# Kernel optimization log

Measured on AMD Instinct MI355X. Metric: run time of the kernel, lower is better.

The kernel has to match this reference:

```python
import jax, jax.numpy as jnp
import numpy as np

B, A, E, H = 512, 4, 10, 256
OBS, PHY, G, MV = 2, 3, 3, 2
T = 10
STEP = 0.05


def setup_inputs() -> dict:
    key = jax.random.key(0)
    ks = jax.random.split(key, 16)
    rn = lambda k, s, sc=1.0: jax.random.normal(k, s, jnp.float32) * sc
    W = 0.1  # weight scale so tanh/sigmoid stay in sane range
    return {
        'observations': rn(ks[0], (B, A, E, OBS)),
        'physical': rn(ks[1], (B, E, PHY)),
        'observed_goals': rn(ks[2], (B, A, G)),
        'mem_physical': jnp.zeros((B, A, E, H), jnp.float32),
        'mem_action': jnp.zeros((B, A, H), jnp.float32),
        'W_ih_p': rn(ks[3], (3 * H, OBS + PHY), W),
        'W_hh_p': rn(ks[4], (3 * H, H), W),
        'b_ih_p': jnp.zeros((3 * H,), jnp.float32),
        'b_hh_p': jnp.zeros((3 * H,), jnp.float32),
        'W_fc_p': rn(ks[5], (H, H), W),
        'b_fc_p': jnp.zeros((H,), jnp.float32),
        'W_ih_a': rn(ks[6], (3 * H, H + G), W),
        'W_hh_a': rn(ks[7], (3 * H, H), W),
        'b_ih_a': jnp.zeros((3 * H,), jnp.float32),
        'b_hh_a': jnp.zeros((3 * H,), jnp.float32),
        'W_fc_a': rn(ks[8], (H, H), W),
        'b_fc_a': jnp.zeros((H,), jnp.float32),
        'W_m1': rn(ks[9], (H, H), W),
        'b_m1': jnp.zeros((H,), jnp.float32),
        'W_m2': rn(ks[10], (MV, H), W),
        'b_m2': jnp.zeros((MV,), jnp.float32),
    }


def _gru(x, h, Wih, Whh, bih, bhh):
    # torch.nn.GRUCell math, vectorized over leading dims
    gi = x @ Wih.T + bih
    gh = h @ Whh.T + bhh
    ir, iz, inn = jnp.split(gi, 3, axis=-1)
    hr, hz, hn = jnp.split(gh, 3, axis=-1)
    r = jax.nn.sigmoid(ir + hr)
    z = jax.nn.sigmoid(iz + hz)
    n = jnp.tanh(inn + r * hn)
    return (1.0 - z) * n + z * h


def reference(observations, physical, observed_goals, mem_physical, mem_action,
              W_ih_p, W_hh_p, b_ih_p, b_hh_p, W_fc_p, b_fc_p,
              W_ih_a, W_hh_a, b_ih_a, b_hh_a, W_fc_a, b_fc_a,
              W_m1, b_m1, W_m2, b_m2):
    b, a, e, _ = observations.shape
    # per-(agent, entity) input: cat(observation, entity physical features)
    phys_b = jnp.broadcast_to(physical[:, None], (b, a, e, physical.shape[-1]))
    x_p = jnp.concatenate([observations, phys_b], axis=-1)  # [B,A,E,5]

    def step(carry, _):
        mp, ma = carry  # [B,A,E,H], [B,A,H]
        # physical ProcessingModule over all (agent, entity) pairs at once
        h_p = _gru(x_p, mp, W_ih_p, W_hh_p, b_ih_p, b_hh_p)          # new 'physical' memory
        proc = jax.nn.elu(h_p @ W_fc_p.T + b_fc_p)                    # [B,A,E,H]
        feat = jnp.max(proc, axis=2)                                  # AdaptiveMaxPool2d((1,H)) over entities
        # ActionModule: GRU over cat(pooled physical feat, observed goal)
        x_a = jnp.concatenate([feat, observed_goals], axis=-1)       # [B,A,H+G]
        h_a = _gru(x_a, ma, W_ih_a, W_hh_a, b_ih_a, b_hh_a)          # new 'action' memory
        proc_a = jax.nn.elu(h_a @ W_fc_a.T + b_fc_a)
        mv = jnp.tanh(jax.nn.elu(proc_a @ W_m1.T + b_m1) @ W_m2.T + b_m2) * STEP  # [B,A,MV]
        return (h_p, h_a), mv

    _, movements = jax.lax.scan(step, (mem_physical, mem_action), None, length=T)
    return movements  # [T,B,A,MV]
```

## Files before the change

kernel.cpp:

```cpp
#include <hip/hip_runtime.h>
#include <math.h>

#define H 256
#define G3 768
#define BB 512
#define AA 4
#define EE 10
#define RP (BB*AA*EE)
#define RA (BB*AA)
#define TT 10
#define NMV 2
#define STEPSC 0.05f
#define DST 260
#define A1B 128
#define A2B 256
#define A3B 128
#define COMB 1280

typedef __attribute__((ext_vector_type(8))) short short8;
typedef __attribute__((ext_vector_type(8))) _Float16 half8;
typedef __attribute__((ext_vector_type(4))) float f32x4;

#if defined(__has_builtin)
#  if __has_builtin(__builtin_amdgcn_global_load_lds)
#    define HAS_GLL 1
#  endif
#endif

__device__ __forceinline__ float sigmoid_(float x){ return 1.f/(1.f + __expf(-x)); }
__device__ __forceinline__ float tanh_(float x){
    float ax = fabsf(x);
    float e  = __expf(-2.f*ax);
    float t  = (1.f - e)/(1.f + e);
    return copysignf(t, x);
}
__device__ __forceinline__ float elu_(float x){ return x > 0.f ? x : (__expf(x) - 1.f); }

#define MFMA16(A,B,C) __builtin_amdgcn_mfma_f32_16x16x32_f16(A,B,C,0,0,0)

__device__ __forceinline__ void cp16(const void* g, void* l) {
#ifdef HAS_GLL
    __builtin_amdgcn_global_load_lds(
        (const __attribute__((address_space(1))) unsigned int*)g,
        (__attribute__((address_space(3))) unsigned int*)l, 16, 0, 0);
#else
    *(short8*)l = *(const short8*)g;
#endif
}

__global__ void k_splitw(const float* __restrict__ src, _Float16* __restrict__ dst,
                         int n, int ldsrc)
{
    int i = blockIdx.x*256 + threadIdx.x;
    if (i < n) {
        int j  = i & 7;
        int l  = (i >> 3) & 63;
        int kc = (i >> 9) & 7;
        int c  = i >> 12;
        int row = c*16 + (l & 15);
        int k   = kc*32 + (l >> 4)*8 + j;
        dst[i] = (_Float16)src[(size_t)row*ldsrc + k];
    }
}

__global__ void k_gia_goal(const float* __restrict__ goals,
                           const float* __restrict__ Wiha,
                           const float* __restrict__ biha,
                           _Float16* __restrict__ out)
{
    int idx = blockIdx.x*256 + threadIdx.x;
    int ra = idx / G3, k = idx % G3;
    float g0 = goals[ra*3+0], g1 = goals[ra*3+1], g2 = goals[ra*3+2];
    const float* w = Wiha + (size_t)k*259 + 256;
    out[idx] = (_Float16)(biha[k] + g0*w[0] + g1*w[1] + g2*w[2]);
}

__global__ void k_cvt(const float* __restrict__ src, _Float16* __restrict__ dst, int n)
{
    int i = blockIdx.x*256 + threadIdx.x;
    if (i < n) dst[i] = (_Float16)src[i];
}

__global__ __launch_bounds__(256, 2)
void k_step(int gru_t, int fc_t, int a1_t, int a2_t, int a3_t,
            _Float16* __restrict__ hp0, _Float16* __restrict__ hp1,
            _Float16* __restrict__ proc0, _Float16* __restrict__ proc1,
            _Float16* __restrict__ ha0, _Float16* __restrict__ ha1,
            _Float16* __restrict__ pca0, _Float16* __restrict__ pca1,
            const _Float16* __restrict__ wWhh, const _Float16* __restrict__ wWfc,
            const _Float16* __restrict__ wWhha, const _Float16* __restrict__ wWiha,
            const _Float16* __restrict__ wWfca, const _Float16* __restrict__ wWm1,
            const _Float16* __restrict__ gia,
            const float* __restrict__ obs, const float* __restrict__ phys,
            const float* __restrict__ Wih, const float* __restrict__ bih,
            const float* __restrict__ bhh, const float* __restrict__ bfcp,
            const float* __restrict__ bhha, const float* __restrict__ bfca,
            const float* __restrict__ bm1,
            const float* __restrict__ Wm2, const float* __restrict__ bm2,
            float* __restrict__ out)
{
    __shared__ char smem[24576];
    int b = blockIdx.x;
    const int tid = threadIdx.x;
    const int wv = tid >> 6, lane = tid & 63;
    const int quad = lane >> 4, l16 = lane & 15;

    if (b < A1B) {
        if (a1_t < 0) return;
        float* D = (float*)smem;
        const _Float16* proc = (a1_t & 1) ? proc1 : proc0;
        const _Float16* hain = (a1_t & 1) ? ha1 : ha0;
        _Float16*      haout = (a1_t & 1) ? ha0 : ha1;
        const int ra0 = b*16;

        for (int i = tid; i < 16*32; i += 256) {
            int r = i >> 5, cg = (i & 31)*8;
            const _Float16* p = proc + ((size_t)(ra0 + r)*EE)*H + cg;
            half8 v = *(const half8*)p;
            float m[8];
            #pragma unroll
            for (int j = 0; j < 8; j++) m[j] = (float)v[j];
            #pragma unroll
            for (int e = 1; e < EE; e++) {
                half8 u = *(const half8*)(p + (size_t)e*H);
                #pragma unroll
                for (int j = 0; j < 8; j++) m[j] = fmaxf(m[j], (float)u[j]);
            }
            #pragma unroll
            for (int j = 0; j < 8; j++) D[r*DST + cg + j] = m[j];
        }
        __syncthreads();

        half8 Fh[8], Hh[8];
        #pragma unroll
        for (int kc = 0; kc < 8; kc++) {
            const float* fp = &D[l16*DST + quad*8 + kc*32];
            #pragma unroll
            for (int j = 0; j < 8; j++) Fh[kc][j] = (_Float16)fp[j];
            Hh[kc] = *(const half8*)(hain + (size_t)(ra0 + l16)*H + quad*8 + kc*32);
        }

        #pragma unroll
        for (int p = 0; p < 2; p++) {
            f32x4 gh[3][2], gx[3][2];
            #pragma unroll
            for (int g = 0; g < 3; g++)
                #pragma unroll
                for (int ch = 0; ch < 2; ch++) {
                    gh[g][ch] = (f32x4){0.f,0.f,0.f,0.f};
                    gx[g][ch] = (f32x4){0.f,0.f,0.f,0.f};
                }
            #pragma unroll
            for (int kc = 0; kc < 8; kc++)
                #pragma unroll
                for (int ch = 0; ch < 2; ch++)
                    #pragma unroll
                    for (int g = 0; g < 3; g++) {
                        const size_t cg = (size_t)(g*16 + wv*4 + p*2 + ch);
                        half8 bh = *(const half8*)(wWhha + (cg*8+kc)*512 + lane*8);
                        half8 bx = *(const half8*)(wWiha + (cg*8+kc)*512 + lane*8);
                        gh[g][ch] = MFMA16(Hh[kc], bh, gh[g][ch]);
                        gx[g][ch] = MFMA16(Fh[kc], bx, gx[g][ch]);
                    }
            #pragma unroll
            for (int ch = 0; ch < 2; ch++) {
                const int c = wv*64 + (p*2+ch)*16 + l16;
                const float br = bhha[c], bz = bhha[256+c], bn = bhha[512+c];
                #pragma unroll
                for (int reg = 0; reg < 4; reg++) {
                    const int r = quad*4 + reg;
                    const _Float16* gp = gia + (size_t)(ra0 + r)*G3;
                    float rg = sigmoid_((float)gp[c]     + gx[0][ch][reg] + gh[0][ch][reg] + br);
                    float z  = sigmoid_((float)gp[256+c] + gx[1][ch][reg] + gh[1][ch][reg] + bz);
                    float n  = tanh_((float)gp[512+c] + gx[2][ch][reg] + rg*(gh[2][ch][reg] + bn));
                    size_t idx = (size_t)(ra0 + r)*H + c;
                    float hprev = (float)hain[idx];
                    haout[idx] = (_Float16)((1.f - z)*n + z*hprev);
                }
            }
        }
        return;
    }
    b -= A1B;

    if (b < A2B) {
        if (a2_t < 0) return;
        const _Float16* hnew = (a2_t & 1) ? ha0 : ha1;
        _Float16*       pca  = (a2_t & 1) ? pca1 : pca0;
        const int ra0 = (b >> 1)*16;
        const int half = b & 1;

        half8 Hh[8];
        #pragma unroll
        for (int kc = 0; kc < 8; kc++)
            Hh[kc] = *(const half8*)(hnew + (size_t)(ra0 + l16)*H + quad*8 + kc*32);

        f32x4 ac[2];
        ac[0] = (f32x4){0.f,0.f,0.f,0.f};
        ac[1] = (f32x4){0.f,0.f,0.f,0.f};
        #pragma unroll
        for (int kc = 0; kc < 8; kc++)
            #pragma unroll
            for (int ch = 0; ch < 2; ch++) {
                const size_t cidx = (size_t)(half*8 + wv*2 + ch);
                half8 w = *(const half8*)(wWfca + (cidx*8+kc)*512 + lane*8);
                ac[ch] = MFMA16(Hh[kc], w, ac[ch]);
            }
        #pragma unroll
        for (int ch = 0; ch < 2; ch++) {
            const int c = (half*8 + wv*2 + ch)*16 + l16;
            const float bs = bfca[c];
            #pragma unroll
            for (int reg = 0; reg < 4; reg++) {
                int row = ra0 + quad*4 + reg;
                pca[(size_t)row*H + c] = (_Float16)elu_(ac[ch][reg] + bs);
            }
        }
        return;
    }
    b -= A2B;

    if (b < A3B) {
        if (a3_t < 0) return;
        float* D = (float*)smem;
        const _Float16* pca = (a3_t & 1) ? pca1 : pca0;
        const int ra0 = b*16;

        half8 Ph[8];
        #pragma unroll
        for (int kc = 0; kc < 8; kc++)
            Ph[kc] = *(const half8*)(pca + (size_t)(ra0 + l16)*H + quad*8 + kc*32);

        f32x4 ac[4];
        #pragma unroll
        for (int ch = 0; ch < 4; ch++) ac[ch] = (f32x4){0.f,0.f,0.f,0.f};
        #pragma unroll
        for (int kc = 0; kc < 8; kc++)
            #pragma unroll
            for (int ch = 0; ch < 4; ch++) {
                half8 w = *(const half8*)(wWm1 + ((size_t)(wv*4+ch)*8+kc)*512 + lane*8);
                ac[ch] = MFMA16(Ph[kc], w, ac[ch]);
            }
        #pragma unroll
        for (int ch = 0; ch < 4; ch++) {
            const int c = wv*64 + ch*16 + l16;
            const float bs = bm1[c];
            #pragma unroll
            for (int reg = 0; reg < 4; reg++)
                D[(quad*4+reg)*DST + c] = elu_(ac[ch][reg] + bs);
        }
        __syncthreads();

        if (tid < 32) {
            int r = tid >> 1, v = tid & 1;
            const float* w = Wm2 + (size_t)v*H;
            float s = bm2[v];
            #pragma unroll 4
            for (int i = 0; i < H/4; i++) {
                float4 a = *(const float4*)&D[r*DST + i*4];
                float4 c = *(const float4*)&w[i*4];
                s = fmaf(a.x,c.x,s); s = fmaf(a.y,c.y,s);
                s = fmaf(a.z,c.z,s); s = fmaf(a.w,c.w,s);
            }
            out[((size_t)a3_t*RA + ra0 + r)*NMV + v] = tanh_(s)*STEPSC;
        }
        return;
    }
    b -= A3B;

    {
        const bool do_gru = (gru_t >= 0);
        const bool do_fc  = (fc_t >= 0);
        if (!do_gru && !do_fc) return;
        _Float16* Bw = (_Float16*)smem;
        const int par = do_gru ? (gru_t & 1) : ((fc_t + 1) & 1);
        const _Float16* hin  = par ? hp1 : hp0;
        _Float16*       hout = par ? hp0 : hp1;
        _Float16*       pout = (fc_t & 1) ? proc1 : proc0;
        const int xm = b % 160, ys = b / 160;
        const int mt0 = xm*128 + wv*16;
        const int mt1 = mt0 + 64;

        half8 Ah[2][8];
        #pragma unroll
        for (int kc = 0; kc < 8; kc++) {
            Ah[0][kc] = *(const half8*)(hin + (size_t)(mt0 + l16)*H + quad*8 + kc*32);
            Ah[1][kc] = *(const half8*)(hin + (size_t)(mt1 + l16)*H + quad*8 + kc*32);
        }

        if (do_gru) {
            for (int s = 0; s < 2; s++) {
                const int cs = ys*2 + s;
                if (s) __syncthreads();
                #pragma unroll
                for (int k = 0; k < 6; k++) {
                    int i = tid + 256*k;
                    int g = i >> 9;
                    cp16(wWhh + (size_t)(g*16+cs)*4096 + (i & 511)*8, &Bw[(size_t)i*8]);
                }
                __syncthreads();

                f32x4 acc[2][3];
                #pragma unroll
                for (int mt = 0; mt < 2; mt++)
                    #pragma unroll
                    for (int g = 0; g < 3; g++) acc[mt][g] = (f32x4){0.f,0.f,0.f,0.f};
                #pragma unroll
                for (int kc = 0; kc < 8; kc++)
                    #pragma unroll
                    for (int g = 0; g < 3; g++) {
                        half8 w = *(const half8*)&Bw[(g*8 + kc)*512 + lane*8];
                        acc[0][g] = MFMA16(Ah[0][kc], w, acc[0][g]);
                        acc[1][g] = MFMA16(Ah[1][kc], w, acc[1][g]);
                    }

                const int col = cs*16 + l16;
                const float bhr = bhh[col], bhz = bhh[256+col], bhn = bhh[512+col];
                const float br_ = bih[col], bz_ = bih[256+col], bn_ = bih[512+col];
                const float* pr = Wih + (size_t)col*5;
                const float* pz = Wih + (size_t)(256+col)*5;
                const float* pn = Wih + (size_t)(512+col)*5;
                #pragma unroll
                for (int mt = 0; mt < 2; mt++) {
                    const int mb = mt ? mt1 : mt0;
                    #pragma unroll
                    for (int r = 0; r < 4; r++) {
                        int row = mb + quad*4 + r;
                        float2 ob = *(const float2*)(obs + (size_t)row*2);
                        int bb = row / (AA*EE), e = row % EE;
                        const float* pp = phys + (size_t)(bb*EE + e)*3;
                        float xv0 = ob.x, xv1 = ob.y, xv2 = pp[0], xv3 = pp[1], xv4 = pp[2];
                        float gr = br_, gz = bz_, gn = bn_;
                        gr = fmaf(xv0,pr[0],gr); gr = fmaf(xv1,pr[1],gr); gr = fmaf(xv2,pr[2],gr);
                        gr = fmaf(xv3,pr[3],gr); gr = fmaf(xv4,pr[4],gr);
                        gz = fmaf(xv0,pz[0],gz); gz = fmaf(xv1,pz[1],gz); gz = fmaf(xv2,pz[2],gz);
                        gz = fmaf(xv3,pz[3],gz); gz = fmaf(xv4,pz[4],gz);
                        gn = fmaf(xv0,pn[0],gn); gn = fmaf(xv1,pn[1],gn); gn = fmaf(xv2,pn[2],gn);
                        gn = fmaf(xv3,pn[3],gn); gn = fmaf(xv4,pn[4],gn);
                        float rg = sigmoid_(gr + acc[mt][0][r] + bhr);
                        float z  = sigmoid_(gz + acc[mt][1][r] + bhz);
                        float n  = tanh_(gn + rg*(acc[mt][2][r] + bhn));
                        size_t idx = (size_t)row*H + col;
                        float hprev = (float)hin[idx];
                        hout[idx] = (_Float16)((1.f - z)*n + z*hprev);
                    }
                }
            }
        }

        if (do_fc) {
            const int cs2 = ys;
            __syncthreads();
            #pragma unroll
            for (int k = 0; k < 4; k++) {
                int i = tid + 256*k;
                cp16(wWfc + (size_t)cs2*8192 + i*8, &Bw[(size_t)i*8]);
            }
            __syncthreads();

            f32x4 acc[2][2];
            #pragma unroll
            for (int mt = 0; mt < 2; mt++)
                #pragma unroll
                for (int ni = 0; ni < 2; ni++) acc[mt][ni] = (f32x4){0.f,0.f,0.f,0.f};
            #pragma unroll
            for (int kc = 0; kc < 8; kc++)
                #pragma unroll
                for (int ni = 0; ni < 2; ni++) {
                    half8 w = *(const half8*)&Bw[ni*4096 + kc*512 + lane*8];
                    acc[0][ni] = MFMA16(Ah[0][kc], w, acc[0][ni]);
                    acc[1][ni] = MFMA16(Ah[1][kc], w, acc[1][ni]);
                }
            #pragma unroll
            for (int mt = 0; mt < 2; mt++) {
                const int mb = mt ? mt1 : mt0;
                #pragma unroll
                for (int ni = 0; ni < 2; ni++) {
                    const int col = cs2*32 + ni*16 + l16;
                    const float bs = bfcp[col];
                    #pragma unroll
                    for (int r = 0; r < 4; r++) {
                        int row = mb + quad*4 + r;
                        pout[(size_t)row*H + col] = (_Float16)elu_(acc[mt][ni][r] + bs);
                    }
                }
            }
        }
    }
}

extern "C" void kernel_launch(void* const* d_in, const int* in_sizes, int n_in,
                              void* d_out, int out_size, void* d_ws, size_t ws_size,
                              hipStream_t stream)
{
    const float* obs  = (const float*)d_in[0];
    const float* phys = (const float*)d_in[1];
    const float* goals= (const float*)d_in[2];
    const float* memp = (const float*)d_in[3];
    const float* mema = (const float*)d_in[4];
    const float* Wihp = (const float*)d_in[5];
    const float* Whhp = (const float*)d_in[6];
    const float* bihp = (const float*)d_in[7];
    const float* bhhp = (const float*)d_in[8];
    const float* Wfcp = (const float*)d_in[9];
    const float* bfcp = (const float*)d_in[10];
    const float* Wiha = (const float*)d_in[11];
    const float* Whha = (const float*)d_in[12];
    const float* biha = (const float*)d_in[13];
    const float* bhha = (const float*)d_in[14];
    const float* Wfca = (const float*)d_in[15];
    const float* bfca = (const float*)d_in[16];
    const float* Wm1  = (const float*)d_in[17];
    const float* bm1  = (const float*)d_in[18];
    const float* Wm2  = (const float*)d_in[19];
    const float* bm2  = (const float*)d_in[20];
    float* out = (float*)d_out;
    (void)ws_size;

    char* base = (char*)d_ws;
    size_t off = 0;
    auto alloc = [&](size_t bytes) -> char* {
        char* p = base + off;
        off += (bytes + 255) & ~(size_t)255;
        return p;
    };
    _Float16* wp_whh = (_Float16*)alloc((size_t)G3*H*2);
    _Float16* wp_wfc = (_Float16*)alloc((size_t)H*H*2);
    _Float16* wa_whh = (_Float16*)alloc((size_t)G3*H*2);
    _Float16* wa_wih = (_Float16*)alloc((size_t)G3*H*2);
    _Float16* wa_wfc = (_Float16*)alloc((size_t)H*H*2);
    _Float16* wa_wm1 = (_Float16*)alloc((size_t)H*H*2);
    _Float16* gia    = (_Float16*)alloc((size_t)RA*G3*2);
    _Float16* hp0    = (_Float16*)alloc((size_t)RP*H*2);
    _Float16* hp1    = (_Float16*)alloc((size_t)RP*H*2);
    _Float16* proc0  = (_Float16*)alloc((size_t)RP*H*2);
    _Float16* proc1  = (_Float16*)alloc((size_t)RP*H*2);
    _Float16* ha0    = (_Float16*)alloc((size_t)RA*H*2);
    _Float16* ha1    = (_Float16*)alloc((size_t)RA*H*2);
    _Float16* pca0   = (_Float16*)alloc((size_t)RA*H*2);
    _Float16* pca1   = (_Float16*)alloc((size_t)RA*H*2);

    k_splitw<<<(G3*H+255)/256, 256, 0, stream>>>(Whhp, wp_whh, G3*H, H);
    k_splitw<<<(H*H+255)/256, 256, 0, stream>>>(Wfcp, wp_wfc, H*H, H);
    k_splitw<<<(G3*H+255)/256, 256, 0, stream>>>(Whha, wa_whh, G3*H, H);
    k_splitw<<<(G3*H+255)/256, 256, 0, stream>>>(Wiha, wa_wih, G3*H, 259);
    k_splitw<<<(H*H+255)/256, 256, 0, stream>>>(Wfca, wa_wfc, H*H, H);
    k_splitw<<<(H*H+255)/256, 256, 0, stream>>>(Wm1,  wa_wm1, H*H, H);
    k_gia_goal<<<RA*G3/256, 256, 0, stream>>>(goals, Wiha, biha, gia);
    k_cvt<<<((size_t)RP*H+255)/256, 256, 0, stream>>>(memp, hp0, RP*H);
    k_cvt<<<((size_t)RA*H+255)/256, 256, 0, stream>>>(mema, ha0, RA*H);

    const int NB = A1B + A2B + A3B + COMB;
    for (int L = 0; L <= TT + 3; L++) {
        int gru_t = (L <= TT-1) ? L : -1;
        int fc_t  = (L-1 >= 0 && L-1 <= TT-1) ? L-1 : -1;
        int a1_t  = (L-2 >= 0 && L-2 <= TT-1) ? L-2 : -1;
        int a2_t  = (L-3 >= 0 && L-3 <= TT-1) ? L-3 : -1;
        int a3_t  = (L-4 >= 0 && L-4 <= TT-1) ? L-4 : -1;
        k_step<<<NB, 256, 0, stream>>>(gru_t, fc_t, a1_t, a2_t, a3_t,
                                       hp0, hp1, proc0, proc1, ha0, ha1, pca0, pca1,
                                       wp_whh, wp_wfc, wa_whh, wa_wih, wa_wfc, wa_wm1,
                                       gia, obs, phys,
                                       Wihp, bihp, bhhp, bfcp,
                                       bhha, bfca, bm1, Wm2, bm2, out);
    }
}
```

Baseline: 643.1 us.

## Fuse action-module FC and MLP stages into the action GRU blocks

The action GRU blocks now keep the new action hidden state in LDS and immediately compute the FC, the first MLP layer and the movement output in the same block. This removes the separate A2/A3 block ranges, the pca global buffers and two pipeline stages, so the launch count drops from 14 to 12. The cost is a longer serial chain inside the 128 action blocks, extra __syncthreads, and more shared memory per block, which may reduce occupancy.

```diff
diff --git a/kernel.cpp b/kernel.cpp
--- a/kernel.cpp
+++ b/kernel.cpp
@@ -12,9 +12,8 @@
 #define NMV 2
 #define STEPSC 0.05f
 #define DST 260
+#define HS 264
 #define A1B 128
-#define A2B 256
-#define A3B 128
 #define COMB 1280
 
 typedef __attribute__((ext_vector_type(8))) short short8;
@@ -82,11 +81,10 @@
 }
 
 __global__ __launch_bounds__(256, 2)
-void k_step(int gru_t, int fc_t, int a1_t, int a2_t, int a3_t,
+void k_step(int gru_t, int fc_t, int a1_t,
             _Float16* __restrict__ hp0, _Float16* __restrict__ hp1,
             _Float16* __restrict__ proc0, _Float16* __restrict__ proc1,
             _Float16* __restrict__ ha0, _Float16* __restrict__ ha1,
-            _Float16* __restrict__ pca0, _Float16* __restrict__ pca1,
             const _Float16* __restrict__ wWhh, const _Float16* __restrict__ wWfc,
             const _Float16* __restrict__ wWhha, const _Float16* __restrict__ wWiha,
             const _Float16* __restrict__ wWfca, const _Float16* __restrict__ wWm1,
@@ -99,7 +97,7 @@
             const float* __restrict__ Wm2, const float* __restrict__ bm2,
             float* __restrict__ out)
 {
-    __shared__ char smem[24576];
+    __shared__ char smem[33536];
     int b = blockIdx.x;
     const int tid = threadIdx.x;
     const int wv = tid >> 6, lane = tid & 63;
@@ -108,6 +106,8 @@
     if (b < A1B) {
         if (a1_t < 0) return;
         float* D = (float*)smem;
+        _Float16* haT = (_Float16*)(smem + 16640);
+        _Float16* paT = (_Float16*)(smem + 25088);
         const _Float16* proc = (a1_t & 1) ? proc1 : proc0;
         const _Float16* hain = (a1_t & 1) ? ha1 : ha0;
         _Float16*      haout = (a1_t & 1) ? ha0 : ha1;
@@ -175,71 +175,53 @@
                     float n  = tanh_((float)gp[512+c] + gx[2][ch][reg] + rg*(gh[2][ch][reg] + bn));
                     size_t idx = (size_t)(ra0 + r)*H + c;
                     float hprev = (float)hain[idx];
-                    haout[idx] = (_Float16)((1.f - z)*n + z*hprev);
-                }
-            }
-        }
-        return;
-    }
-    b -= A1B;
-
-    if (b < A2B) {
-        if (a2_t < 0) return;
-        const _Float16* hnew = (a2_t & 1) ? ha0 : ha1;
-        _Float16*       pca  = (a2_t & 1) ? pca1 : pca0;
-        const int ra0 = (b >> 1)*16;
-        const int half = b & 1;
-
-        half8 Hh[8];
+                    float hv = (1.f - z)*n + z*hprev;
+                    haout[idx] = (_Float16)hv;
+                    haT[r*HS + c] = (_Float16)hv;
+                }
+            }
+        }
+        __syncthreads();
+
+        half8 Hh2[8];
         #pragma unroll
         for (int kc = 0; kc < 8; kc++)
-            Hh[kc] = *(const half8*)(hnew + (size_t)(ra0 + l16)*H + quad*8 + kc*32);
-
-        f32x4 ac[2];
-        ac[0] = (f32x4){0.f,0.f,0.f,0.f};
-        ac[1] = (f32x4){0.f,0.f,0.f,0.f};
+            Hh2[kc] = *(const half8*)(haT + l16*HS + quad*8 + kc*32);
+
+        f32x4 ac2[4];
+        #pragma unroll
+        for (int ch = 0; ch < 4; ch++) ac2[ch] = (f32x4){0.f,0.f,0.f,0.f};
         #pragma unroll
         for (int kc = 0; kc < 8; kc++)
             #pragma unroll
-            for (int ch = 0; ch < 2; ch++) {
-                const size_t cidx = (size_t)(half*8 + wv*2 + ch);
-                half8 w = *(const half8*)(wWfca + (cidx*8+kc)*512 + lane*8);
-                ac[ch] = MFMA16(Hh[kc], w, ac[ch]);
-            }
-        #pragma unroll
-        for (int ch = 0; ch < 2; ch++) {
-            const int c = (half*8 + wv*2 + ch)*16 + l16;
+            for (int ch = 0; ch < 4; ch++) {
+                half8 w = *(const half8*)(wWfca + ((size_t)(wv*4+ch)*8+kc)*512 + lane*8);
+                ac2[ch] = MFMA16(Hh2[kc], w, ac2[ch]);
+            }
+        #pragma unroll
+        for (int ch = 0; ch < 4; ch++) {
+            const int c = (wv*4+ch)*16 + l16;
             const float bs = bfca[c];
             #pragma unroll
-            for (int reg = 0; reg < 4; reg++) {
-                int row = ra0 + quad*4 + reg;
-                pca[(size_t)row*H + c] = (_Float16)elu_(ac[ch][reg] + bs);
-            }
-        }
-        return;
-    }
-    b -= A2B;
-
-    if (b < A3B) {
-        if (a3_t < 0) return;
-        float* D = (float*)smem;
-        const _Float16* pca = (a3_t & 1) ? pca1 : pca0;
-        const int ra0 = b*16;
+            for (int reg = 0; reg < 4; reg++)
+                paT[(quad*4+reg)*HS + c] = (_Float16)elu_(ac2[ch][reg] + bs);
+        }
+        __syncthreads();
 
         half8 Ph[8];
         #pragma unroll
         for (int kc = 0; kc < 8; kc++)
-            Ph[kc] = *(const half8*)(pca + (size_t)(ra0 + l16)*H + quad*8 + kc*32);
-
-        f32x4 ac[4];
-        #pragma unroll
-        for (int ch = 0; ch < 4; ch++) ac[ch] = (f32x4){0.f,0.f,0.f,0.f};
+            Ph[kc] = *(const half8*)(paT + l16*HS + quad*8 + kc*32);
+
+        f32x4 ac3[4];
+        #pragma unroll
+        for (int ch = 0; ch < 4; ch++) ac3[ch] = (f32x4){0.f,0.f,0.f,0.f};
         #pragma unroll
         for (int kc = 0; kc < 8; kc++)
             #pragma unroll
             for (int ch = 0; ch < 4; ch++) {
                 half8 w = *(const half8*)(wWm1 + ((size_t)(wv*4+ch)*8+kc)*512 + lane*8);
-                ac[ch] = MFMA16(Ph[kc], w, ac[ch]);
+                ac3[ch] = MFMA16(Ph[kc], w, ac3[ch]);
             }
         #pragma unroll
         for (int ch = 0; ch < 4; ch++) {
@@ -247,7 +229,7 @@
             const float bs = bm1[c];
             #pragma unroll
             for (int reg = 0; reg < 4; reg++)
-                D[(quad*4+reg)*DST + c] = elu_(ac[ch][reg] + bs);
+                D[(quad*4+reg)*DST + c] = elu_(ac3[ch][reg] + bs);
         }
         __syncthreads();
 
@@ -262,11 +244,11 @@
                 s = fmaf(a.x,c.x,s); s = fmaf(a.y,c.y,s);
                 s = fmaf(a.z,c.z,s); s = fmaf(a.w,c.w,s);
             }
-            out[((size_t)a3_t*RA + ra0 + r)*NMV + v] = tanh_(s)*STEPSC;
+            out[((size_t)a1_t*RA + ra0 + r)*NMV + v] = tanh_(s)*STEPSC;
         }
         return;
     }
-    b -= A3B;
+    b -= A1B;
 
     {
         const bool do_gru = (gru_t >= 0);
@@ -437,8 +419,6 @@
     _Float16* proc1  = (_Float16*)alloc((size_t)RP*H*2);
     _Float16* ha0    = (_Float16*)alloc((size_t)RA*H*2);
     _Float16* ha1    = (_Float16*)alloc((size_t)RA*H*2);
-    _Float16* pca0   = (_Float16*)alloc((size_t)RA*H*2);
-    _Float16* pca1   = (_Float16*)alloc((size_t)RA*H*2);
 
     k_splitw<<<(G3*H+255)/256, 256, 0, stream>>>(Whhp, wp_whh, G3*H, H);
     k_splitw<<<(H*H+255)/256, 256, 0, stream>>>(Wfcp, wp_wfc, H*H, H);
@@ -450,15 +430,13 @@
     k_cvt<<<((size_t)RP*H+255)/256, 256, 0, stream>>>(memp, hp0, RP*H);
     k_cvt<<<((size_t)RA*H+255)/256, 256, 0, stream>>>(mema, ha0, RA*H);
 
-    const int NB = A1B + A2B + A3B + COMB;
-    for (int L = 0; L <= TT + 3; L++) {
+    const int NB = A1B + COMB;
+    for (int L = 0; L <= TT + 1; L++) {
         int gru_t = (L <= TT-1) ? L : -1;
         int fc_t  = (L-1 >= 0 && L-1 <= TT-1) ? L-1 : -1;
         int a1_t  = (L-2 >= 0 && L-2 <= TT-1) ? L-2 : -1;
-        int a2_t  = (L-3 >= 0 && L-3 <= TT-1) ? L-3 : -1;
-        int a3_t  = (L-4 >= 0 && L-4 <= TT-1) ? L-4 : -1;
-        k_step<<<NB, 256, 0, stream>>>(gru_t, fc_t, a1_t, a2_t, a3_t,
-                                       hp0, hp1, proc0, proc1, ha0, ha1, pca0, pca1,
+        k_step<<<NB, 256, 0, stream>>>(gru_t, fc_t, a1_t,
+                                       hp0, hp1, proc0, proc1, ha0, ha1,
                                        wp_whh, wp_wfc, wa_whh, wa_wih, wa_wfc, wa_wm1,
                                        gia, obs, phys,
                                        Wihp, bihp, bhhp, bfcp,
```

Result: slower. 785.0 us (+22.1%).
